# Performance work log

Measured on AMD Instinct MI355X. Metric: run time of the kernel, lower is better.

Reference implementation:

```python
import jax, jax.numpy as jnp
import numpy as np

# Static graph-batch geometry: B graphs, N nodes each (contiguous), DEG avg degree.
B, N, DEG = 128, 512, 16
GID, GH = 128, 128      # g_in_dim, g_hidden_dim
CID, CE = 64, 64        # c_in_dim, c_embed_dim
HAZ = 256               # haz_dim
K1, K2, K3 = 256, 128, 64


def _gcn(x, src, dst, mask, W, b, n):
    # GCN layer with self loops over masked (surviving) nodes; masked-out nodes contribute nothing.
    h = x @ W  # [n, GH]
    w = mask[src] * mask[dst]                                  # edge alive iff both endpoints alive
    deg = mask + jax.ops.segment_sum(w, dst, num_segments=n)    # +mask = self loop
    dinv = jax.lax.rsqrt(jnp.maximum(deg, 1.0))
    norm = w * dinv[src] * dinv[dst]
    agg = jax.ops.segment_sum(norm[:, None] * h[src], dst, num_segments=n)
    self_term = h * (mask * dinv * dinv)[:, None]               # self-loop norm = 1/deg
    return (agg + self_term + b) * mask[:, None]


def _pool(x, mask, p, k):
    # Score-based top-k pooling (MVPool score -> gate -> keep top ratio per graph), mask-based for static shapes.
    score = jax.nn.sigmoid((x @ p) / jnp.sqrt(jnp.sum(p * p)))  # [B*N]
    s = jnp.where(mask > 0, score, -jnp.inf).reshape(B, N)
    _, idx = jax.lax.top_k(s, k)                                 # [B, k]
    new_mask = jnp.zeros((B, N), x.dtype).at[jnp.arange(B)[:, None], idx].set(1.0).reshape(-1)
    x = x * (score * new_mask)[:, None]
    return x, new_mask


def _readout(x, mask):
    # readout='both': concat(global_max_pool, global_mean_pool) per graph.
    xm = x.reshape(B, N, -1)
    m = mask.reshape(B, N, 1)
    mx = jnp.max(jnp.where(m > 0, xm, -1e30), axis=1)
    avg = jnp.sum(xm * m, axis=1) / jnp.maximum(jnp.sum(m, axis=1), 1.0)
    return jnp.concatenate([mx, avg], axis=1)


def _forward(x, inp_c, src, dst, W1, b1, W2, b2, W3, b3, p1, p2, p3, We, Wa, ba, Wb, bb, Wc):
    n = B * N
    mask = jnp.ones((n,), x.dtype)
    x = jax.nn.relu(_gcn(x, src, dst, mask, W1, b1, n))
    x, mask = _pool(x, mask, p1, K1)
    x1 = _readout(x, mask)
    x = jax.nn.relu(_gcn(x, src, dst, mask, W2, b2, n))
    x, mask = _pool(x, mask, p2, K2)
    x2 = _readout(x, mask)
    x = jax.nn.relu(_gcn(x, src, dst, mask, W3, b3, n))
    x, mask = _pool(x, mask, p3, K3)
    x3 = _readout(x, mask)
    hg = jax.nn.relu(x1) + jax.nn.relu(x2) + jax.nn.relu(x3)     # [B, 2*GH]
    embed = jax.nn.relu(inp_c @ We)                               # [B, CE]
    fusion = jnp.concatenate([embed, hg], axis=1)                 # [B, 320]
    h = jax.nn.relu(fusion @ Wa + ba)                             # dropout skipped (eval mode)
    h = jax.nn.relu(h @ Wb + bb)
    return h @ Wc                                                 # out_dim=1 -> Identity


def setup_inputs() -> dict:
    key = jax.random.key(0)
    ks = jax.random.split(key, 16)
    n = B * N
    x = jax.random.normal(ks[0], (n, GID), jnp.float32)
    inp_c = jax.random.normal(ks[1], (B, CID), jnp.float32)
    offs = (jnp.arange(B, dtype=jnp.int32) * N)[:, None]
    src = (jax.random.randint(ks[2], (B, N * DEG), 0, N, jnp.int32) + offs).reshape(-1)
    dst = (jax.random.randint(ks[3], (B, N * DEG), 0, N, jnp.int32) + offs).reshape(-1)
    edge_index = jnp.stack([src, dst])
    batch = jnp.arange(n, dtype=jnp.int32) // N
    def lin(k, i, o):
        return jax.random.normal(k, (i, o), jnp.float32) / np.float32(np.sqrt(i))
    return dict(
        x=x, inp_c=inp_c, edge_index=edge_index, batch=batch,
        W1=lin(ks[4], GID, GH), b1=jnp.zeros((GH,), jnp.float32),
        W2=lin(ks[5], GH, GH), b2=jnp.zeros((GH,), jnp.float32),
        W3=lin(ks[6], GH, GH), b3=jnp.zeros((GH,), jnp.float32),
        p1=jax.random.normal(ks[7], (GH,), jnp.float32),
        p2=jax.random.normal(ks[8], (GH,), jnp.float32),
        p3=jax.random.normal(ks[9], (GH,), jnp.float32),
        We=lin(ks[10], CID, CE),
        Wa=lin(ks[11], 2 * GH + CE, HAZ), ba=jnp.zeros((HAZ,), jnp.float32),
        Wb=lin(ks[12], HAZ, HAZ // 2), bb=jnp.zeros((HAZ // 2,), jnp.float32),
        Wc=lin(ks[13], HAZ // 2, 1),
    )


def reference(x, inp_c, edge_index, batch, W1, b1, W2, b2, W3, b3, p1, p2, p3, We, Wa, ba, Wb, bb, Wc):
    # batch is implicitly arange(n)//N (contiguous equal-size graphs); reductions use the reshape form.
    src, dst = edge_index[0], edge_index[1]
    return _forward(x, inp_c, src, dst, W1, b1, W2, b2, W3, b3, p1, p2, p3, We, Wa, ba, Wb, bb, Wc)
```

## Files before the change

kernel.cpp:

```cpp
#include <hip/hip_runtime.h>
#include <math.h>

#define NNODE 65536
#define NEDGE 1048576
#define NGRAPH 128
#define NPG 512
#define EPG 8192

typedef _Float16 f16x8 __attribute__((ext_vector_type(8)));
typedef _Float16 f16x4 __attribute__((ext_vector_type(4)));
typedef float f32x4 __attribute__((ext_vector_type(4)));


__global__ __launch_bounds__(512) void k_csr(const int* __restrict__ srcE, const int* __restrict__ dstE,
                                             int* __restrict__ rp, int* __restrict__ csr,
                                             float* __restrict__ gate, int* __restrict__ alive,
                                             float* __restrict__ dinv) {
    __shared__ int cnt[512];
    __shared__ int tmp[512];
    int g = blockIdx.x, t = threadIdx.x;
    int nd = g * NPG + t;
    cnt[t] = 0;
    gate[nd] = 1.f;
    alive[nd] = nd;
    __syncthreads();
    int ebase = g * EPG;
    int dl[16];
    for (int i = 0; i < 16; ++i) {
        int e = ebase + t + i * 512;
        int d = dstE[e] - g * NPG;
        dl[i] = d;
        atomicAdd(&cnt[d], 1);
    }
    __syncthreads();
    int v = cnt[t], incl = v;
    dinv[nd] = rsqrtf(1.f + (float)v);
    for (int off = 1; off < 512; off <<= 1) {
        tmp[t] = incl; __syncthreads();
        if (t >= off) incl += tmp[t - off];
        __syncthreads();
    }
    int excl = incl - v;
    rp[nd] = ebase + excl;
    if (g == NGRAPH - 1 && t == 511) rp[NNODE] = NEDGE;
    __syncthreads();
    cnt[t] = excl;
    __syncthreads();
    for (int i = 0; i < 16; ++i) {
        int e = ebase + t + i * 512;
        int pos = atomicAdd(&cnt[dl[i]], 1);
        csr[ebase + pos] = srcE[e];
    }
}


__global__ __launch_bounds__(256) void k_wconv(const float* __restrict__ W0, const float* __restrict__ W1,
                                               const float* __restrict__ W2, _Float16* __restrict__ wh,
                                               _Float16* __restrict__ wl) {
    int l = blockIdx.x >> 6;
    int e = (blockIdx.x & 63) * 256 + threadIdx.x;
    const float* W = (l == 0) ? W0 : (l == 1) ? W1 : W2;
    int k = e >> 7, n = e & 127;
    float w = W[e];
    _Float16 hi = (_Float16)w;
    _Float16 lo = (_Float16)((w - (float)hi) * 2048.0f);
    int nt = n >> 4, nn = n & 15, ks = k >> 5, quad = (k & 31) >> 3, j = k & 7;
    int off = l * 16384 + ((nt * 4 + ks) * 64 + (quad * 16 + nn)) * 8 + j;
    wh[off] = hi;
    wl[off] = lo;
}


__global__ __launch_bounds__(192) void k_pnorm(const float* __restrict__ p0, const float* __restrict__ p1,
                                               const float* __restrict__ p2, float* __restrict__ qinv) {
    int w = threadIdx.x >> 6, lane = threadIdx.x & 63;
    const float* P = (w == 0) ? p0 : (w == 1) ? p1 : p2;
    float s = P[lane] * P[lane] + P[lane + 64] * P[lane + 64];
    for (int m = 32; m >= 1; m >>= 1) s += __shfl_xor(s, m);
    if (lane == 0) qinv[w] = rsqrtf(s);
}


#define CVT8(hi8, lo8, a0, a1, a2, a3, a4, a5, a6, a7)                         \
    {                                                                           \
        _Float16 q0 = (_Float16)a0, q1 = (_Float16)a1, q2 = (_Float16)a2,       \
                 q3 = (_Float16)a3, q4 = (_Float16)a4, q5 = (_Float16)a5,       \
                 q6 = (_Float16)a6, q7 = (_Float16)a7;                          \
        hi8 = (f16x8){q0, q1, q2, q3, q4, q5, q6, q7};                          \
        lo8 = (f16x8){(_Float16)((a0 - (float)q0) * 2048.f),                    \
                      (_Float16)((a1 - (float)q1) * 2048.f),                    \
                      (_Float16)((a2 - (float)q2) * 2048.f),                    \
                      (_Float16)((a3 - (float)q3) * 2048.f),                    \
                      (_Float16)((a4 - (float)q4) * 2048.f),                    \
                      (_Float16)((a5 - (float)q5) * 2048.f),                    \
                      (_Float16)((a6 - (float)q6) * 2048.f),                    \
                      (_Float16)((a7 - (float)q7) * 2048.f)};                   \
    }

__global__ __launch_bounds__(256, 2) void k_gemm(const float* __restrict__ x0, const _Float16* __restrict__ xh,
                                                 const _Float16* __restrict__ xl, const _Float16* __restrict__ wh,
                                                 const _Float16* __restrict__ wl, const float* __restrict__ gate,
                                                 const int* __restrict__ alive, float* __restrict__ h,
                                                 int srcF32, int perg) {
    __shared__ _Float16 aH[128 * 72];
    __shared__ _Float16 aL[128 * 72];
    __shared__ _Float16 bH[8192];
    __shared__ _Float16 bL[8192];
    int t = threadIdx.x;
    int lane = t & 63;
    int wv = t >> 6;
    int quad = lane >> 4, mm = lane & 15;
    int gg = blockIdx.x & 127;
    int cc0 = blockIdx.x >> 7;
    int rowbase = gg * perg + cc0 * 128;

    f32x4 accH[2][8], accM[2][8];
    for (int a = 0; a < 2; ++a)
        for (int b = 0; b < 8; ++b) {
            accH[a][b] = (f32x4){0.f, 0.f, 0.f, 0.f};
            accM[a][b] = (f32x4){0.f, 0.f, 0.f, 0.f};
        }

    for (int kh = 0; kh < 2; ++kh) {
        if (kh) __syncthreads();
        for (int pp = 0; pp < 4; ++pp) {
            int seg = t + pp * 256;
            int nt = seg >> 7, ksl = (seg >> 6) & 1, ln = seg & 63;
            int goff = ((nt * 4 + kh * 2 + ksl) * 64 + ln) * 8;
            *(uint4*)(bH + seg * 8) = *(const uint4*)(wh + goff);
            *(uint4*)(bL + seg * 8) = *(const uint4*)(wl + goff);
        }
        for (int pp = 0; pp < 4; ++pp) {
            int c = t + pp * 256;
            int r = c >> 3, ch = c & 7;
            int node = alive[rowbase + r];
            size_t src = (size_t)node * 128 + kh * 64 + ch * 8;
            f16x8 hi8, lo8;
            if (srcF32) {
                float4 v0 = *(const float4*)(x0 + src);
                float4 v1 = *(const float4*)(x0 + src + 4);
                CVT8(hi8, lo8, v0.x, v0.y, v0.z, v0.w, v1.x, v1.y, v1.z, v1.w);
            } else {
                hi8 = *(const f16x8*)(xh + src);
                lo8 = *(const f16x8*)(xl + src);
            }
            *(f16x8*)(aH + r * 72 + ch * 8) = hi8;
            *(f16x8*)(aL + r * 72 + ch * 8) = lo8;
        }
        __syncthreads();

        for (int ksl = 0; ksl < 2; ++ksl) {
            f16x8 Ah[2], Al[2];
            for (int mt = 0; mt < 2; ++mt) {
                int row = wv * 32 + mt * 16 + mm;
                Ah[mt] = *(const f16x8*)(aH + row * 72 + ksl * 32 + quad * 8);
                Al[mt] = *(const f16x8*)(aL + row * 72 + ksl * 32 + quad * 8);
            }
            for (int nt = 0; nt < 8; ++nt) {
                f16x8 Bh = *(const f16x8*)(bH + ((nt * 2 + ksl) * 64 + lane) * 8);
                f16x8 Bl = *(const f16x8*)(bL + ((nt * 2 + ksl) * 64 + lane) * 8);
                for (int mt = 0; mt < 2; ++mt) {
                    accH[mt][nt] = __builtin_amdgcn_mfma_f32_16x16x32_f16(Ah[mt], Bh, accH[mt][nt], 0, 0, 0);
                    accM[mt][nt] = __builtin_amdgcn_mfma_f32_16x16x32_f16(Ah[mt], Bl, accM[mt][nt], 0, 0, 0);
                    accM[mt][nt] = __builtin_amdgcn_mfma_f32_16x16x32_f16(Al[mt], Bh, accM[mt][nt], 0, 0, 0);
                }
            }
        }
    }

    for (int mt = 0; mt < 2; ++mt)
        for (int i = 0; i < 4; ++i) {
            int rl = wv * 32 + mt * 16 + quad * 4 + i;
            int node = alive[rowbase + rl];
            float g = gate[node];
            float* hr = h + (size_t)node * 128 + mm;
            for (int nt = 0; nt < 8; ++nt)
                hr[nt * 16] = g * (accH[mt][nt][i] + accM[mt][nt][i] * (1.f / 2048.f));
        }
}


__global__ __launch_bounds__(512) void k_agg(const float* __restrict__ h, const float* __restrict__ dinv,
                                             const int* __restrict__ rp, const int* __restrict__ csr,
                                             const int* __restrict__ alive, const float* __restrict__ bias,
                                             const float* __restrict__ p, _Float16* __restrict__ xh,
                                             _Float16* __restrict__ xl, float* __restrict__ spart, int Kp) {
    __shared__ float hsl[512 * 68];
    __shared__ float dinv_l[512];
    __shared__ float2 nbw[32][16];
    __shared__ float bias_l[64];
    __shared__ float p_l[64];
    int t = threadIdx.x;
    int g = blockIdx.x & 127;
    int fh = blockIdx.x >> 7;
    int fb = fh * 64;
    int gbase = g * NPG;

    for (int r0 = 0; r0 < 512; r0 += 64) {
        int r = r0 + (t >> 3);
        int f8 = (t & 7) * 8;
        const float* src = h + (size_t)(gbase + r) * 128 + fb + f8;
        float4 v0 = *(const float4*)(src);
        float4 v1 = *(const float4*)(src + 4);
        *(float4*)(hsl + r * 68 + f8) = v0;
        *(float4*)(hsl + r * 68 + f8 + 4) = v1;
    }
    dinv_l[t] = dinv[gbase + t];
    if (t < 64) { bias_l[t] = bias[fb + t]; p_l[t] = p[fb + t]; }
    __syncthreads();

    int lane16 = t & 15;
    int qid = t >> 4;

    for (int idx = qid; idx < Kp; idx += 32) {
        int d = alive[g * Kp + idx];
        int rd = d - gbase;
        int jb = rp[d], je = rp[d + 1];
        float dvd = dinv_l[rd];
        float4 hd = *(const float4*)(hsl + rd * 68 + lane16 * 4);
        float4 acc;
        acc.x = dvd * hd.x; acc.y = dvd * hd.y; acc.z = dvd * hd.z; acc.w = dvd * hd.w;

        for (int bk = jb; bk < je; bk += 16) {
            int nk = je - bk; if (nk > 16) nk = 16;
            float wv = 0.f;
            int rs = rd;
            if (lane16 < nk) {
                rs = csr[bk + lane16] - gbase;
                wv = dinv_l[rs];
            }
            nbw[qid][lane16] = make_float2(wv, __int_as_float(rs));
            int nk4 = (nk + 3) & ~3;
            for (int k = 0; k < nk4; k += 4) {
                float2 e0 = nbw[qid][k];
                float2 e1 = nbw[qid][k + 1];
                float2 e2 = nbw[qid][k + 2];
                float2 e3 = nbw[qid][k + 3];
                float4 h0 = *(const float4*)(hsl + __float_as_int(e0.y) * 68 + lane16 * 4);
                float4 h1 = *(const float4*)(hsl + __float_as_int(e1.y) * 68 + lane16 * 4);
                float4 h2 = *(const float4*)(hsl + __float_as_int(e2.y) * 68 + lane16 * 4);
                float4 h3 = *(const float4*)(hsl + __float_as_int(e3.y) * 68 + lane16 * 4);
                acc.x = fmaf(e0.x, h0.x, acc.x); acc.y = fmaf(e0.x, h0.y, acc.y);
                acc.z = fmaf(e0.x, h0.z, acc.z); acc.w = fmaf(e0.x, h0.w, acc.w);
                acc.x = fmaf(e1.x, h1.x, acc.x); acc.y = fmaf(e1.x, h1.y, acc.y);
                acc.z = fmaf(e1.x, h1.z, acc.z); acc.w = fmaf(e1.x, h1.w, acc.w);
                acc.x = fmaf(e2.x, h2.x, acc.x); acc.y = fmaf(e2.x, h2.y, acc.y);
                acc.z = fmaf(e2.x, h2.z, acc.z); acc.w = fmaf(e2.x, h2.w, acc.w);
                acc.x = fmaf(e3.x, h3.x, acc.x); acc.y = fmaf(e3.x, h3.y, acc.y);
                acc.z = fmaf(e3.x, h3.z, acc.z); acc.w = fmaf(e3.x, h3.w, acc.w);
            }
        }

        float4 b4 = *(const float4*)(bias_l + lane16 * 4);
        float4 o;
        o.x = fmaxf(fmaf(dvd, acc.x, b4.x), 0.f);
        o.y = fmaxf(fmaf(dvd, acc.y, b4.y), 0.f);
        o.z = fmaxf(fmaf(dvd, acc.z, b4.z), 0.f);
        o.w = fmaxf(fmaf(dvd, acc.w, b4.w), 0.f);

        _Float16 q0 = (_Float16)o.x, q1 = (_Float16)o.y, q2 = (_Float16)o.z, q3 = (_Float16)o.w;
        f16x4 oh = {q0, q1, q2, q3};
        f16x4 ol = {(_Float16)((o.x - (float)q0) * 2048.f), (_Float16)((o.y - (float)q1) * 2048.f),
                    (_Float16)((o.z - (float)q2) * 2048.f), (_Float16)((o.w - (float)q3) * 2048.f)};
        *(f16x4*)(xh + (size_t)d * 128 + fb + lane16 * 4) = oh;
        *(f16x4*)(xl + (size_t)d * 128 + fb + lane16 * 4) = ol;

        float4 p4 = *(const float4*)(p_l + lane16 * 4);
        float ps = o.x * p4.x + o.y * p4.y + o.z * p4.z + o.w * p4.w;
        ps += __shfl_xor(ps, 1);
        ps += __shfl_xor(ps, 2);
        ps += __shfl_xor(ps, 4);
        ps += __shfl_xor(ps, 8);
        if (lane16 == 0) spart[(size_t)fh * NNODE + d] = ps;
    }
}


__global__ __launch_bounds__(512) void k_pool(const _Float16* __restrict__ xh, const _Float16* __restrict__ xl,
                                              const float* __restrict__ spart, const float* __restrict__ qinv,
                                              int lidx, float* __restrict__ gate,
                                              int* __restrict__ alive, float* __restrict__ hg,
                                              const int* __restrict__ rp, const int* __restrict__ csr,
                                              float* __restrict__ dinv, int K, int last) {
    __shared__ unsigned hist[1024];
    __shared__ unsigned wsum[8];
    __shared__ float cand[512];
    __shared__ int ad[256];
    __shared__ float ag[256];
    __shared__ float red[1024];
    __shared__ int m_new[512];
    __shared__ int scnt;
    __shared__ unsigned ccnt;
    __shared__ unsigned tbb, tbab;
    __shared__ float thrS;
    int t = threadIdx.x, g = blockIdx.x;
    int gbase = g * NPG;
    int d = gbase + t;

    float odv = dinv[d];
    int m = odv > 0.f;
    float z = spart[d] + spart[NNODE + d];
    float sc = 1.f / (1.f + expf(-z * qinv[lidx]));
    unsigned bits = m ? __float_as_uint(sc) : 0u;
    unsigned bucket = bits >> 21;
    hist[t] = 0; hist[t + 512] = 0;
    if (t == 0) { scnt = 0; ccnt = 0; }
    __syncthreads();
    atomicAdd(&hist[bucket], 1u);
    __syncthreads();
    unsigned a0 = hist[1023 - 2 * t];
    unsigned a1 = hist[1022 - 2 * t];
    unsigned pair = a0 + a1;
    unsigned v = pair;
    for (int o = 1; o < 64; o <<= 1) {
        unsigned n = __shfl_up(v, o);
        if ((t & 63) >= o) v += n;
    }
    if ((t & 63) == 63) wsum[t >> 6] = v;
    __syncthreads();
    if (t == 0) {
        unsigned run = 0;
        for (int i = 0; i < 8; ++i) { unsigned x = wsum[i]; wsum[i] = run; run += x; }
    }
    __syncthreads();
    unsigned incl = v + wsum[t >> 6];
    unsigned excl = incl - pair;
    unsigned uK = (unsigned)K;
    if (excl < uK && excl + a0 >= uK) { tbb = 1023 - 2 * t; tbab = excl; }
    else if (excl + a0 < uK && incl >= uK) { tbb = 1022 - 2 * t; tbab = excl + a0; }
    __syncthreads();
    unsigned bsel = tbb;
    unsigned r = uK - tbab;
    if (m && bucket == bsel) {
        unsigned pos = atomicAdd(&ccnt, 1u);
        cand[pos] = sc;
    }
    __syncthreads();
    unsigned c = ccnt;
    if (t < (int)c) {
        float vv = cand[t];
        unsigned gt = 0;
        for (unsigned i = 0; i < c; ++i) gt += (cand[i] > vv) ? 1u : 0u;
        if (gt == r - 1) thrS = vv;
    }
    __syncthreads();
    float thr = thrS;

    int nm = (m && sc >= thr) ? 1 : 0;
    gate[d] = nm ? sc : 0.f;
    m_new[t] = nm;
    if (nm) {
        int pos = atomicAdd(&scnt, 1);
        if (pos < K) {
            alive[g * K + pos] = d;
            ad[pos] = d;
            ag[pos] = sc;
        }
    }
    __syncthreads();

    if (!last) {
        float nd = 0.f;
        if (nm) {
            int jb = rp[d], je = rp[d + 1];
            int sum = 0;
            for (int j = jb; j < je; ++j) sum += m_new[csr[j] - gbase];
            nd = rsqrtf(1.f + (float)sum);
        }
        dinv[d] = nd;
    }

    int f = t & 127, c2 = t >> 7;
    float mx = 0.f, sm = 0.f;
#define REC(node) ((float)xh[(size_t)(node)*128 + f] + (float)xl[(size_t)(node)*128 + f] * (1.f / 2048.f))
    for (int j = c2; j < K; j += 16) {
        float v0 = REC(ad[j]) * ag[j];
        float v1 = REC(ad[j + 4]) * ag[j + 4];
        float v2 = REC(ad[j + 8]) * ag[j + 8];
        float v3 = REC(ad[j + 12]) * ag[j + 12];
        mx = fmaxf(fmaxf(fmaxf(mx, v0), fmaxf(v1, v2)), v3);
        sm += v0 + v1 + v2 + v3;
    }
#undef REC
    red[t] = mx; red[512 + t] = sm;
    __syncthreads();
    if (c2 == 0) {
        for (int cc = 1; cc < 4; ++cc) {
            mx = fmaxf(mx, red[cc * 128 + f]);
            sm += red[512 + cc * 128 + f];
        }
        hg[g * 256 + f] += mx;
        hg[g * 256 + 128 + f] += sm / (float)K;
    }
}


__global__ __launch_bounds__(256) void k_mlp(const float* __restrict__ inp_c, const float* __restrict__ hg,
                                             const float* __restrict__ We, const float* __restrict__ Wa,
                                             const float* __restrict__ ba, const float* __restrict__ Wb,
                                             const float* __restrict__ bb, const float* __restrict__ Wc,
                                             float* __restrict__ out) {
    __shared__ float fus[320];
    __shared__ float h1[256];
    __shared__ float h2[128];
    int t = threadIdx.x, g = blockIdx.x;
    if (t < 64) {
        float a = 0.f;
        for (int j = 0; j < 64; ++j) a = fmaf(inp_c[g * 64 + j], We[j * 64 + t], a);
        fus[t] = fmaxf(a, 0.f);
    }
    fus[64 + t] = hg[g * 256 + t];
    __syncthreads();
    {
        float a = ba[t];
        for (int j = 0; j < 320; ++j) a = fmaf(fus[j], Wa[j * 256 + t], a);
        h1[t] = fmaxf(a, 0.f);
    }
    __syncthreads();
    if (t < 128) {
        float a = bb[t];
        for (int j = 0; j < 256; ++j) a = fmaf(h1[j], Wb[j * 128 + t], a);
        h2[t] = fmaxf(a, 0.f);
    }
    __syncthreads();
    if (t == 0) {
        float a = 0.f;
        for (int j = 0; j < 128; ++j) a = fmaf(h2[j], Wc[j], a);
        out[g] = a;
    }
}


extern "C" void kernel_launch(void* const* d_in, const int* in_sizes, int n_in,
                              void* d_out, int out_size, void* d_ws, size_t ws_size,
                              hipStream_t stream) {
    (void)in_sizes; (void)n_in; (void)out_size; (void)ws_size;
    const float* x_in  = (const float*)d_in[0];
    const float* inp_c = (const float*)d_in[1];
    const int*   ei    = (const int*)d_in[2];
    const int* srcE = ei;
    const int* dstE = ei + NEDGE;
    const float* Wl[3] = {(const float*)d_in[4], (const float*)d_in[6], (const float*)d_in[8]};
    const float* bl[3] = {(const float*)d_in[5], (const float*)d_in[7], (const float*)d_in[9]};
    const float* Pl[3] = {(const float*)d_in[10], (const float*)d_in[11], (const float*)d_in[12]};
    const float* We = (const float*)d_in[13];
    const float* Wa = (const float*)d_in[14];
    const float* ba = (const float*)d_in[15];
    const float* Wb = (const float*)d_in[16];
    const float* bb = (const float*)d_in[17];
    const float* Wc = (const float*)d_in[18];
    float* out = (float*)d_out;

    char* w = (char*)d_ws;
    size_t off = 0;
    auto alloc = [&](size_t bytes) -> void* {
        void* p = w + off;
        off = (off + bytes + 255) & ~(size_t)255;
        return p;
    };
    int*   rp    = (int*)alloc((NNODE + 1) * 4);
    int*   csr   = (int*)alloc(NEDGE * 4);
    float* dinv  = (float*)alloc(NNODE * 4);
    float* gate  = (float*)alloc(NNODE * 4);
    float* spart = (float*)alloc((size_t)2 * NNODE * 4);
    float* qinv  = (float*)alloc(256);
    int*   alive = (int*)alloc(NNODE * 4);
    float* hbuf  = (float*)alloc((size_t)NNODE * 128 * 4);
    _Float16* xh = (_Float16*)alloc((size_t)NNODE * 128 * 2);
    _Float16* xl = (_Float16*)alloc((size_t)NNODE * 128 * 2);
    float* hg    = (float*)alloc(NGRAPH * 256 * 4);
    _Float16* wfh = (_Float16*)alloc(3 * 16384 * 2);
    _Float16* wfl = (_Float16*)alloc(3 * 16384 * 2);

    hipMemsetAsync(hg, 0, NGRAPH * 256 * 4, stream);
    k_wconv<<<192, 256, 0, stream>>>(Wl[0], Wl[1], Wl[2], wfh, wfl);
    k_pnorm<<<1, 192, 0, stream>>>(Pl[0], Pl[1], Pl[2], qinv);
    k_csr<<<NGRAPH, 512, 0, stream>>>(srcE, dstE, rp, csr, gate, alive, dinv);

    const int rows_in[3] = {65536, 32768, 16384};
    const int Ks[3] = {256, 128, 64};
    const int Kp[3] = {512, 256, 128};
    for (int l = 0; l < 3; ++l) {
        k_gemm<<<rows_in[l] / 128, 256, 0, stream>>>(x_in, xh, xl, wfh + l * 16384, wfl + l * 16384,
                                                     gate, alive, hbuf, l == 0, rows_in[l] / 128);
        k_agg<<<256, 512, 0, stream>>>(hbuf, dinv, rp, csr, alive, bl[l], Pl[l],
                                       xh, xl, spart, Kp[l]);
        k_pool<<<NGRAPH, 512, 0, stream>>>(xh, xl, spart, qinv, l, gate, alive, hg,
                                           rp, csr, dinv, Ks[l], l == 2);
    }
    k_mlp<<<NGRAPH, 256, 0, stream>>>(inp_c, hg, We, Wa, ba, Wb, bb, Wc, out);
}
```

Baseline: 298.9 us.

## Merge setup kernels, warp-scan CSR, and add compact-slab aggregation for pooled layers

Folds the hg memset and the p-norm kernel into existing launches, replaces the shared-memory Hillis-Steele scan in CSR build with a wavefront shuffle scan, and doubles aggregation block size to 1024 threads. For layers 2 and 3 a new aggregation kernel loads only the surviving nodes' features into a smaller LDS slab through a node-to-slot map, instead of staging all 512 rows. The aim is fewer launches and barriers and less global traffic in the pooled layers. The trade-off is larger blocks with higher LDS use, which may lower occupancy.

```diff
diff --git a/kernel.cpp b/kernel.cpp
--- a/kernel.cpp
+++ b/kernel.cpp
@@ -15,14 +15,15 @@
 __global__ __launch_bounds__(512) void k_csr(const int* __restrict__ srcE, const int* __restrict__ dstE,
                                              int* __restrict__ rp, int* __restrict__ csr,
                                              float* __restrict__ gate, int* __restrict__ alive,
-                                             float* __restrict__ dinv) {
+                                             float* __restrict__ dinv, float* __restrict__ hg) {
     __shared__ int cnt[512];
-    __shared__ int tmp[512];
+    __shared__ int wsum[8];
     int g = blockIdx.x, t = threadIdx.x;
     int nd = g * NPG + t;
     cnt[t] = 0;
     gate[nd] = 1.f;
     alive[nd] = nd;
+    if (t < 256) hg[g * 256 + t] = 0.f;
     __syncthreads();
     int ebase = g * EPG;
     int dl[16];
@@ -33,17 +34,25 @@
         atomicAdd(&cnt[d], 1);
     }
     __syncthreads();
-    int v = cnt[t], incl = v;
+    int v = cnt[t];
     dinv[nd] = rsqrtf(1.f + (float)v);
-    for (int off = 1; off < 512; off <<= 1) {
-        tmp[t] = incl; __syncthreads();
-        if (t >= off) incl += tmp[t - off];
-        __syncthreads();
-    }
+    int lane = t & 63, wid = t >> 6;
+    int x = v;
+    for (int o = 1; o < 64; o <<= 1) {
+        int n = __shfl_up(x, o);
+        if (lane >= o) x += n;
+    }
+    if (lane == 63) wsum[wid] = x;
+    __syncthreads();
+    if (t == 0) {
+        int run = 0;
+        for (int i = 0; i < 8; ++i) { int s = wsum[i]; wsum[i] = run; run += s; }
+    }
+    __syncthreads();
+    int incl = x + wsum[wid];
     int excl = incl - v;
     rp[nd] = ebase + excl;
     if (g == NGRAPH - 1 && t == 511) rp[NNODE] = NEDGE;
-    __syncthreads();
     cnt[t] = excl;
     __syncthreads();
     for (int i = 0; i < 16; ++i) {
@@ -54,9 +63,22 @@
 }
 
 
-__global__ __launch_bounds__(256) void k_wconv(const float* __restrict__ W0, const float* __restrict__ W1,
+__global__ __launch_bounds__(256) void k_setup(const float* __restrict__ W0, const float* __restrict__ W1,
                                                const float* __restrict__ W2, _Float16* __restrict__ wh,
-                                               _Float16* __restrict__ wl) {
+                                               _Float16* __restrict__ wl,
+                                               const float* __restrict__ p0, const float* __restrict__ p1,
+                                               const float* __restrict__ p2, float* __restrict__ qinv) {
+    if (blockIdx.x == 192) {
+        int t = threadIdx.x;
+        if (t < 192) {
+            int w = t >> 6, lane = t & 63;
+            const float* P = (w == 0) ? p0 : (w == 1) ? p1 : p2;
+            float s = P[lane] * P[lane] + P[lane + 64] * P[lane + 64];
+            for (int m = 32; m >= 1; m >>= 1) s += __shfl_xor(s, m);
+            if (lane == 0) qinv[w] = rsqrtf(s);
+        }
+        return;
+    }
     int l = blockIdx.x >> 6;
     int e = (blockIdx.x & 63) * 256 + threadIdx.x;
     const float* W = (l == 0) ? W0 : (l == 1) ? W1 : W2;
@@ -68,16 +90,6 @@
     int off = l * 16384 + ((nt * 4 + ks) * 64 + (quad * 16 + nn)) * 8 + j;
     wh[off] = hi;
     wl[off] = lo;
-}
-
-
-__global__ __launch_bounds__(192) void k_pnorm(const float* __restrict__ p0, const float* __restrict__ p1,
-                                               const float* __restrict__ p2, float* __restrict__ qinv) {
-    int w = threadIdx.x >> 6, lane = threadIdx.x & 63;
-    const float* P = (w == 0) ? p0 : (w == 1) ? p1 : p2;
-    float s = P[lane] * P[lane] + P[lane + 64] * P[lane + 64];
-    for (int m = 32; m >= 1; m >>= 1) s += __shfl_xor(s, m);
-    if (lane == 0) qinv[w] = rsqrtf(s);
 }
 
 
@@ -180,14 +192,14 @@
 }
 
 
-__global__ __launch_bounds__(512) void k_agg(const float* __restrict__ h, const float* __restrict__ dinv,
-                                             const int* __restrict__ rp, const int* __restrict__ csr,
-                                             const int* __restrict__ alive, const float* __restrict__ bias,
-                                             const float* __restrict__ p, _Float16* __restrict__ xh,
-                                             _Float16* __restrict__ xl, float* __restrict__ spart, int Kp) {
+__global__ __launch_bounds__(1024) void k_aggL(const float* __restrict__ h, const float* __restrict__ dinv,
+                                               const int* __restrict__ rp, const int* __restrict__ csr,
+                                               const int* __restrict__ alive, const float* __restrict__ bias,
+                                               const float* __restrict__ p, _Float16* __restrict__ xh,
+                                               _Float16* __restrict__ xl, float* __restrict__ spart, int Kp) {
     __shared__ float hsl[512 * 68];
     __shared__ float dinv_l[512];
-    __shared__ float2 nbw[32][16];
+    __shared__ float2 nbw[64][16];
     __shared__ float bias_l[64];
     __shared__ float p_l[64];
     int t = threadIdx.x;
@@ -196,7 +208,7 @@
     int fb = fh * 64;
     int gbase = g * NPG;
 
-    for (int r0 = 0; r0 < 512; r0 += 64) {
+    for (int r0 = 0; r0 < 512; r0 += 128) {
         int r = r0 + (t >> 3);
         int f8 = (t & 7) * 8;
         const float* src = h + (size_t)(gbase + r) * 128 + fb + f8;
@@ -205,14 +217,14 @@
         *(float4*)(hsl + r * 68 + f8) = v0;
         *(float4*)(hsl + r * 68 + f8 + 4) = v1;
     }
-    dinv_l[t] = dinv[gbase + t];
+    if (t < 512) dinv_l[t] = dinv[gbase + t];
     if (t < 64) { bias_l[t] = bias[fb + t]; p_l[t] = p[fb + t]; }
     __syncthreads();
 
     int lane16 = t & 15;
     int qid = t >> 4;
 
-    for (int idx = qid; idx < Kp; idx += 32) {
+    for (int idx = qid; idx < Kp; idx += 64) {
         int d = alive[g * Kp + idx];
         int rd = d - gbase;
         int jb = rp[d], je = rp[d + 1];
@@ -276,6 +288,109 @@
 }
 
 
+__global__ __launch_bounds__(1024) void k_aggS(const float* __restrict__ h, const float* __restrict__ dinv,
+                                               const int* __restrict__ rp, const int* __restrict__ csr,
+                                               const int* __restrict__ alive, const float* __restrict__ bias,
+                                               const float* __restrict__ p, _Float16* __restrict__ xh,
+                                               _Float16* __restrict__ xl, float* __restrict__ spart, int Kp) {
+    __shared__ float slab[256 * 68];
+    __shared__ float dinv_l[512];
+    __shared__ int   map_l[512];
+    __shared__ float2 nbw[64][16];
+    __shared__ float bias_l[64];
+    __shared__ float p_l[64];
+    int t = threadIdx.x;
+    int g = blockIdx.x & 127;
+    int fh = blockIdx.x >> 7;
+    int fb = fh * 64;
+    int gbase = g * NPG;
+
+    if (t < 512) { dinv_l[t] = dinv[gbase + t]; map_l[t] = 0; }
+    if (t < 64) { bias_l[t] = bias[fb + t]; p_l[t] = p[fb + t]; }
+    for (int r0 = 0; r0 < Kp; r0 += 128) {
+        int r = r0 + (t >> 3);
+        if (r < Kp) {
+            int node = alive[g * Kp + r];
+            int f8 = (t & 7) * 8;
+            const float* src = h + (size_t)node * 128 + fb + f8;
+            float4 v0 = *(const float4*)(src);
+            float4 v1 = *(const float4*)(src + 4);
+            *(float4*)(slab + r * 68 + f8) = v0;
+            *(float4*)(slab + r * 68 + f8 + 4) = v1;
+        }
+    }
+    __syncthreads();
+    if (t < Kp) map_l[alive[g * Kp + t] - gbase] = t;
+    __syncthreads();
+
+    int lane16 = t & 15;
+    int qid = t >> 4;
+
+    for (int idx = qid; idx < Kp; idx += 64) {
+        int d = alive[g * Kp + idx];
+        int rd = d - gbase;
+        int jb = rp[d], je = rp[d + 1];
+        float dvd = dinv_l[rd];
+        float4 hd = *(const float4*)(slab + idx * 68 + lane16 * 4);
+        float4 acc;
+        acc.x = dvd * hd.x; acc.y = dvd * hd.y; acc.z = dvd * hd.z; acc.w = dvd * hd.w;
+
+        for (int bk = jb; bk < je; bk += 16) {
+            int nk = je - bk; if (nk > 16) nk = 16;
+            float wv = 0.f;
+            int sl = idx;
+            if (lane16 < nk) {
+                int rs = csr[bk + lane16] - gbase;
+                wv = dinv_l[rs];
+                sl = map_l[rs];
+            }
+            nbw[qid][lane16] = make_float2(wv, __int_as_float(sl));
+            int nk4 = (nk + 3) & ~3;
+            for (int k = 0; k < nk4; k += 4) {
+                float2 e0 = nbw[qid][k];
+                float2 e1 = nbw[qid][k + 1];
+                float2 e2 = nbw[qid][k + 2];
+                float2 e3 = nbw[qid][k + 3];
+                float4 h0 = *(const float4*)(slab + __float_as_int(e0.y) * 68 + lane16 * 4);
+                float4 h1 = *(const float4*)(slab + __float_as_int(e1.y) * 68 + lane16 * 4);
+                float4 h2 = *(const float4*)(slab + __float_as_int(e2.y) * 68 + lane16 * 4);
+                float4 h3 = *(const float4*)(slab + __float_as_int(e3.y) * 68 + lane16 * 4);
+                acc.x = fmaf(e0.x, h0.x, acc.x); acc.y = fmaf(e0.x, h0.y, acc.y);
+                acc.z = fmaf(e0.x, h0.z, acc.z); acc.w = fmaf(e0.x, h0.w, acc.w);
+                acc.x = fmaf(e1.x, h1.x, acc.x); acc.y = fmaf(e1.x, h1.y, acc.y);
+                acc.z = fmaf(e1.x, h1.z, acc.z); acc.w = fmaf(e1.x, h1.w, acc.w);
+                acc.x = fmaf(e2.x, h2.x, acc.x); acc.y = fmaf(e2.x, h2.y, acc.y);
+                acc.z = fmaf(e2.x, h2.z, acc.z); acc.w = fmaf(e2.x, h2.w, acc.w);
+                acc.x = fmaf(e3.x, h3.x, acc.x); acc.y = fmaf(e3.x, h3.y, acc.y);
+                acc.z = fmaf(e3.x, h3.z, acc.z); acc.w = fmaf(e3.x, h3.w, acc.w);
+            }
+        }
+
+        float4 b4 = *(const float4*)(bias_l + lane16 * 4);
+        float4 o;
+        o.x = fmaxf(fmaf(dvd, acc.x, b4.x), 0.f);
+        o.y = fmaxf(fmaf(dvd, acc.y, b4.y), 0.f);
+        o.z = fmaxf(fmaf(dvd, acc.z, b4.z), 0.f);
+        o.w = fmaxf(fmaf(dvd, acc.w, b4.w), 0.f);
+
+        _Float16 q0 = (_Float16)o.x, q1 = (_Float16)o.y, q2 = (_Float16)o.z, q3 = (_Float16)o.w;
+        f16x4 oh = {q0, q1, q2, q3};
+        f16x4 ol = {(_Float16)((o.x - (float)q0) * 2048.f), (_Float16)((o.y - (float)q1) * 2048.f),
+                    (_Float16)((o.z - (float)q2) * 2048.f), (_Float16)((o.w - (float)q3) * 2048.f)};
+        *(f16x4*)(xh + (size_t)d * 128 + fb + lane16 * 4) = oh;
+        *(f16x4*)(xl + (size_t)d * 128 + fb + lane16 * 4) = ol;
+
+        float4 p4 = *(const float4*)(p_l + lane16 * 4);
+        float ps = o.x * p4.x + o.y * p4.y + o.z * p4.z + o.w * p4.w;
+        ps += __shfl_xor(ps, 1);
+        ps += __shfl_xor(ps, 2);
+        ps += __shfl_xor(ps, 4);
+        ps += __shfl_xor(ps, 8);
+        if (lane16 == 0) spart[(size_t)fh * NNODE + d] = ps;
+    }
+}
+
+
 __global__ __launch_bounds__(512) void k_pool(const _Float16* __restrict__ xh, const _Float16* __restrict__ xl,
                                               const float* __restrict__ spart, const float* __restrict__ qinv,
                                               int lidx, float* __restrict__ gate,
@@ -472,10 +587,8 @@
     _Float16* wfh = (_Float16*)alloc(3 * 16384 * 2);
     _Float16* wfl = (_Float16*)alloc(3 * 16384 * 2);
 
-    hipMemsetAsync(hg, 0, NGRAPH * 256 * 4, stream);
-    k_wconv<<<192, 256, 0, stream>>>(Wl[0], Wl[1], Wl[2], wfh, wfl);
-    k_pnorm<<<1, 192, 0, stream>>>(Pl[0], Pl[1], Pl[2], qinv);
-    k_csr<<<NGRAPH, 512, 0, stream>>>(srcE, dstE, rp, csr, gate, alive, dinv);
+    k_setup<<<193, 256, 0, stream>>>(Wl[0], Wl[1], Wl[2], wfh, wfl, Pl[0], Pl[1], Pl[2], qinv);
+    k_csr<<<NGRAPH, 512, 0, stream>>>(srcE, dstE, rp, csr, gate, alive, dinv, hg);
 
     const int rows_in[3] = {65536, 32768, 16384};
     const int Ks[3] = {256, 128, 64};
@@ -483,8 +596,13 @@
     for (int l = 0; l < 3; ++l) {
         k_gemm<<<rows_in[l] / 128, 256, 0, stream>>>(x_in, xh, xl, wfh + l * 16384, wfl + l * 16384,
                                                      gate, alive, hbuf, l == 0, rows_in[l] / 128);
-        k_agg<<<256, 512, 0, stream>>>(hbuf, dinv, rp, csr, alive, bl[l], Pl[l],
-                                       xh, xl, spart, Kp[l]);
+        if (l == 0) {
+            k_aggL<<<256, 1024, 0, stream>>>(hbuf, dinv, rp, csr, alive, bl[l], Pl[l],
+                                             xh, xl, spart, Kp[l]);
+        } else {
+            k_aggS<<<256, 1024, 0, stream>>>(hbuf, dinv, rp, csr, alive, bl[l], Pl[l],
+                                             xh, xl, spart, Kp[l]);
+        }
         k_pool<<<NGRAPH, 512, 0, stream>>>(xh, xl, spart, qinv, l, gate, alive, hg,
                                            rp, csr, dinv, Ks[l], l == 2);
     }
```

After: 272.1 us. -9.0%, faster.
